# Performance work log

Measured on AMD Instinct MI355X. Metric: run time of the kernel, lower is better.

The kernel has to match this reference:

```python
import jax, jax.numpy as jnp
import numpy as np

N, E, H, DE = 50000, 800000, 128, 16

def silu(x):
    return x * jax.nn.sigmoid(x)

def setup_inputs() -> dict:
    key = jax.random.key(0)
    ks = jax.random.split(key, 24)
    def W(k, i, o, s=0.02):
        return (jax.random.normal(k, (i, o), jnp.float32) * s)
    inp = {
        'h': jax.random.normal(ks[0], (N, H), jnp.float32),
        'coord': jax.random.normal(ks[1], (N, 3), jnp.float32),
        'edge_index': jax.random.randint(ks[2], (2, E), 0, N),
        'edge_attr': jax.random.normal(ks[3], (E, DE), jnp.float32),
        # mes_mlp: Linear(2H+1+DE -> H), SiLU, Linear(H -> H), SiLU
        'mes_w1': W(ks[4], 2 * H + 1 + DE, H), 'mes_b1': jnp.zeros((H,), jnp.float32),
        'mes_w2': W(ks[5], H, H),              'mes_b2': jnp.zeros((H,), jnp.float32),
        # edge_mlp: Linear(H+1+DE -> H), SiLU, Linear(H -> H)
        'edge_w1': W(ks[6], H + 1 + DE, H),    'edge_b1': jnp.zeros((H,), jnp.float32),
        'edge_w2': W(ks[7], H, H),             'edge_b2': jnp.zeros((H,), jnp.float32),
        # node_mlp: Linear(H+H -> H), SiLU, Linear(H -> H)
        'node_w1': W(ks[8], 2 * H, H),         'node_b1': jnp.zeros((H,), jnp.float32),
        'node_w2': W(ks[9], H, H),             'node_b2': jnp.zeros((H,), jnp.float32),
        # coord_mlp: Linear(H -> H), SiLU, Linear(H -> 1, no bias, xavier gain 0.001)
        'coord_w1': W(ks[10], H, H),           'coord_b1': jnp.zeros((H,), jnp.float32),
        'coord_w2': W(ks[11], H, 1, s=0.001),
    }
    return inp

def reference(h, coord, edge_index, edge_attr,
              mes_w1, mes_b1, mes_w2, mes_b2,
              edge_w1, edge_b1, edge_w2, edge_b2,
              node_w1, node_b1, node_w2, node_b2,
              coord_w1, coord_b1, coord_w2):
    row, col = edge_index[0], edge_index[1]
    n = h.shape[0]
    # coord2radial
    coord_diff = coord[row] - coord[col]                        # [E,3]
    radial = jnp.sum(coord_diff ** 2, axis=1, keepdims=True)    # [E,1]
    norm = jnp.sqrt(radial + 1e-8)
    coord_diff = coord_diff / (norm + 1.0)
    # mes_model
    mes_in = jnp.concatenate([h[row], h[col], radial, edge_attr], axis=1)
    edge_feat = silu(silu(mes_in @ mes_w1 + mes_b1) @ mes_w2 + mes_b2)  # [E,H]
    # coord_model (agg='sum', no tanh)
    trans = coord_diff * (silu(edge_feat @ coord_w1 + coord_b1) @ coord_w2)  # [E,3]
    coord = coord + jax.ops.segment_sum(trans, col, num_segments=n)
    # node_model (recurrent)
    agg = jax.ops.segment_sum(edge_feat, col, num_segments=n)   # [N,H]
    node_in = jnp.concatenate([h, agg], axis=1)
    h = h + (silu(node_in @ node_w1 + node_b1) @ node_w2 + node_b2)
    # edge_model
    edge_in = jnp.concatenate([edge_feat, radial, edge_attr], axis=1)
    edge_out = silu(edge_in @ edge_w1 + edge_b1) @ edge_w2 + edge_b2
    return (h, coord, edge_out)
```

## Files before the change

kernel.cpp:

```cpp
#include <hip/hip_runtime.h>
#include <cstdint>
#include <cstddef>

typedef float f32x4 __attribute__((ext_vector_type(4)));
typedef __bf16 bf16x8 __attribute__((ext_vector_type(8)));
typedef unsigned short u16;

#define Hdim 128
#define DEdim 16
#define APITCH 296
#define FOFF   136
#define NPITCH 264

__device__ __forceinline__ u16 f2bf(float f){
  uint32_t u = __builtin_bit_cast(uint32_t, f);
  u += 0x7fffu + ((u >> 16) & 1u);
  return (u16)(u >> 16);
}
__device__ __forceinline__ uint32_t pack_bf2(float a, float b){
  return (uint32_t)f2bf(a) | ((uint32_t)f2bf(b) << 16);
}
__device__ __forceinline__ float bf2f(uint32_t lo16){
  return __builtin_bit_cast(float, lo16 << 16);
}
__device__ __forceinline__ float silu_f(float x){
  return x / (1.0f + __expf(-x));
}

template<int KC>
__device__ __forceinline__ void gemm_tile(
    const u16* A, int apitch,
    const u16* __restrict__ Bt, int kpad,
    const float* __restrict__ bias,
    int wv, int cidx, int hi, f32x4 (&acc)[4][2])
{
  const int c0 = (wv*2+0)*16 + cidx;
  const int c1 = (wv*2+1)*16 + cidx;
  const float b0 = bias[c0];
  const float b1 = bias[c1];
  #pragma unroll
  for (int rt=0; rt<4; ++rt){
    acc[rt][0] = (f32x4){b0,b0,b0,b0};
    acc[rt][1] = (f32x4){b1,b1,b1,b1};
  }
  #pragma unroll
  for (int kc=0; kc<KC; ++kc){
    const int ko = kc*32 + hi*8;
    bf16x8 bb0 = *(const bf16x8*)(Bt + (size_t)c0*kpad + ko);
    bf16x8 bb1 = *(const bf16x8*)(Bt + (size_t)c1*kpad + ko);
    #pragma unroll
    for (int rt=0; rt<4; ++rt){
      bf16x8 a = *(const bf16x8*)(A + (rt*16+cidx)*apitch + ko);
      acc[rt][0] = __builtin_amdgcn_mfma_f32_16x16x32_bf16(a, bb0, acc[rt][0], 0,0,0);
      acc[rt][1] = __builtin_amdgcn_mfma_f32_16x16x32_bf16(a, bb1, acc[rt][1], 0,0,0);
    }
  }
}

template<bool GATHER>
__global__ __launch_bounds__(256, 4) void egcl_edge(
    const float* __restrict__ h, const float* __restrict__ coord,
    const int* __restrict__ ei, const float* __restrict__ ea,
    const float* __restrict__ mes_b1, const float* __restrict__ mes_b2,
    const float* __restrict__ edge_b1, const float* __restrict__ edge_b2,
    const float* __restrict__ coord_b1, const float* __restrict__ coord_w2,
    const u16* __restrict__ w_mes1t, const u16* __restrict__ w_mes2t,
    const u16* __restrict__ w_coord1t, const u16* __restrict__ w_edge1t,
    const u16* __restrict__ w_edge2t,
    float* __restrict__ agg, u16* __restrict__ feat,
    float* __restrict__ out_coord, float* __restrict__ out_edge, int E, int N)
{
  __shared__ u16 Ab[64*APITCH];
  __shared__ float cds[64*4];
  __shared__ float tvs[64];
  __shared__ int cnode[64];

  const int tid  = threadIdx.x;
  const int lane = tid & 63;
  const int wv   = tid >> 6;
  const int e0   = blockIdx.x * 64;
  const int cidx = lane & 15;
  const int hi   = lane >> 4;

  {
    const int le   = wv*16 + (lane>>2);
    const int part = lane & 3;
    int eg = e0 + le;
    if (eg >= E) eg = E-1;
    const int node = (part < 2) ? ei[eg] : ei[E + eg];
    const float* src = h + (size_t)node*Hdim + (part&1)*64;
    u16* dst = Ab + le*APITCH + part*64;
    #pragma unroll
    for (int j=0;j<16;++j){
      const float4 v = ((const float4*)src)[j];
      ushort4 o; o.x=f2bf(v.x); o.y=f2bf(v.y); o.z=f2bf(v.z); o.w=f2bf(v.w);
      *(ushort4*)(dst + j*4) = o;
    }
    if (part == 0){
      const int cn = ei[E + eg];
      const float dx = coord[(size_t)node*3+0] - coord[(size_t)cn*3+0];
      const float dy = coord[(size_t)node*3+1] - coord[(size_t)cn*3+1];
      const float dz = coord[(size_t)node*3+2] - coord[(size_t)cn*3+2];
      const float radial = dx*dx + dy*dy + dz*dz;
      const float inv = 1.0f/(sqrtf(radial + 1e-8f) + 1.0f);
      cds[le*4+0]=dx*inv; cds[le*4+1]=dy*inv; cds[le*4+2]=dz*inv; cds[le*4+3]=radial;
      cnode[le] = cn;
      Ab[le*APITCH + 256] = f2bf(radial);
      #pragma unroll
      for (int j=0;j<DEdim;++j)
        Ab[le*APITCH + 257 + j] = f2bf(ea[(size_t)eg*DEdim + j]);
      #pragma unroll
      for (int j=273;j<288;++j) Ab[le*APITCH + j] = 0;
    }
    if (tid < 64) tvs[tid] = 0.f;
  }
  __syncthreads();

  f32x4 acc[4][2];

  gemm_tile<9>(Ab, APITCH, w_mes1t, 288, mes_b1, wv, cidx, hi, acc);
  __syncthreads();
  #pragma unroll
  for (int rt=0; rt<4; ++rt)
    #pragma unroll
    for (int j=0;j<2;++j){
      const int col = (wv*2+j)*16 + cidx;
      #pragma unroll
      for (int i=0;i<4;++i)
        Ab[(rt*16 + hi*4 + i)*APITCH + col] = f2bf(silu_f(acc[rt][j][i]));
    }
  if (tid < 64){
    const int row = tid;
    int eg = e0 + row; if (eg >= E) eg = E-1;
    Ab[row*APITCH + FOFF + 128] = f2bf(cds[row*4+3]);
    const float4* eap = (const float4*)(ea + (size_t)eg*DEdim);
    #pragma unroll
    for (int j=0;j<4;++j){
      const float4 v = eap[j];
      Ab[row*APITCH + FOFF + 129 + j*4 + 0] = f2bf(v.x);
      Ab[row*APITCH + FOFF + 129 + j*4 + 1] = f2bf(v.y);
      Ab[row*APITCH + FOFF + 129 + j*4 + 2] = f2bf(v.z);
      Ab[row*APITCH + FOFF + 129 + j*4 + 3] = f2bf(v.w);
    }
    #pragma unroll
    for (int j=145;j<160;++j) Ab[row*APITCH + FOFF + j] = 0;
  }
  __syncthreads();

  gemm_tile<4>(Ab, APITCH, w_mes2t, 128, mes_b2, wv, cidx, hi, acc);
  #pragma unroll
  for (int rt=0; rt<4; ++rt)
    #pragma unroll
    for (int j=0;j<2;++j){
      const int col = (wv*2+j)*16 + cidx;
      #pragma unroll
      for (int i=0;i<4;++i){
        const int row = rt*16 + hi*4 + i;
        const float v = silu_f(acc[rt][j][i]);
        if (!GATHER && e0 + row < E)
          atomicAdd(agg + (size_t)cnode[row]*Hdim + col, v);
        Ab[row*APITCH + FOFF + col] = f2bf(v);
      }
    }
  __syncthreads();

  if (GATHER){
    const int row = tid >> 2, seg = tid & 3;
    if (e0 + row < E){
      const int4* s = (const int4*)(Ab + row*APITCH + FOFF + seg*32);
      int4* d = (int4*)(feat + (size_t)(e0+row)*Hdim + seg*32);
      d[0]=s[0]; d[1]=s[1]; d[2]=s[2]; d[3]=s[3];
    }
  }

  gemm_tile<4>(Ab + FOFF, APITCH, w_coord1t, 128, coord_b1, wv, cidx, hi, acc);
  {
    const float cw0 = coord_w2[(wv*2+0)*16 + cidx];
    const float cw1 = coord_w2[(wv*2+1)*16 + cidx];
    #pragma unroll
    for (int rt=0; rt<4; ++rt)
      #pragma unroll
      for (int i=0;i<4;++i){
        float p = silu_f(acc[rt][0][i])*cw0 + silu_f(acc[rt][1][i])*cw1;
        p += __shfl_xor(p, 1);
        p += __shfl_xor(p, 2);
        p += __shfl_xor(p, 4);
        p += __shfl_xor(p, 8);
        if (cidx == 0) atomicAdd(&tvs[rt*16 + hi*4 + i], p);
      }
  }
  __syncthreads();
  if (tid < 192){
    const int le = tid/3, d = tid%3;
    if (e0 + le < E)
      atomicAdd(out_coord + (size_t)cnode[le]*3 + d, cds[le*4+d]*tvs[le]);
  }

  gemm_tile<5>(Ab + FOFF, APITCH, w_edge1t, 160, edge_b1, wv, cidx, hi, acc);
  #pragma unroll
  for (int rt=0; rt<4; ++rt)
    #pragma unroll
    for (int j=0;j<2;++j){
      const int col = (wv*2+j)*16 + cidx;
      #pragma unroll
      for (int i=0;i<4;++i)
        Ab[(rt*16 + hi*4 + i)*APITCH + col] = f2bf(silu_f(acc[rt][j][i]));
    }
  __syncthreads();

  gemm_tile<4>(Ab, APITCH, w_edge2t, 128, edge_b2, wv, cidx, hi, acc);
  #pragma unroll
  for (int rt=0; rt<4; ++rt)
    #pragma unroll
    for (int j=0;j<2;++j){
      const int col = (wv*2+j)*16 + cidx;
      #pragma unroll
      for (int i=0;i<4;++i){
        const int row = rt*16 + hi*4 + i;
        const int eg = e0 + row;
        if (eg < E) out_edge[(size_t)eg*Hdim + col] = acc[rt][j][i];
      }
    }
}

template<bool GATHER>
__global__ __launch_bounds__(256, 4) void egcl_node(
    const float* __restrict__ h, const float* __restrict__ agg,
    const int* __restrict__ offs, const int* __restrict__ deg,
    const int* __restrict__ elist, const u16* __restrict__ feat,
    const float* __restrict__ node_b1, const float* __restrict__ node_b2,
    const u16* __restrict__ w_node1t, const u16* __restrict__ w_node2t,
    float* __restrict__ out_h, int N)
{
  __shared__ u16 Ab[64*NPITCH];
  const int tid  = threadIdx.x;
  const int lane = tid & 63;
  const int wv   = tid >> 6;
  const int r0   = blockIdx.x * 64;
  const int cidx = lane & 15;
  const int hi   = lane >> 4;

  {
    const int le   = wv*16 + (lane>>2);
    const int part = lane & 3;
    int g = r0 + le;
    if (g >= N) g = N-1;
    const float* src = h + (size_t)g*Hdim + part*32;
    u16* dst = Ab + le*NPITCH + part*32;
    #pragma unroll
    for (int j=0;j<8;++j){
      const float4 v = ((const float4*)src)[j];
      ushort4 o; o.x=f2bf(v.x); o.y=f2bf(v.y); o.z=f2bf(v.z); o.w=f2bf(v.w);
      *(ushort4*)(dst + j*4) = o;
    }
  }
  if (GATHER){
    const uint32_t* fp = (const uint32_t*)feat;
    for (int ln=0; ln<16; ++ln){
      const int le = wv*16 + ln;
      const int g = r0 + le;
      float a0 = 0.f, a1 = 0.f;
      if (g < N){
        const int start = __builtin_amdgcn_readfirstlane(offs[g]);
        const int dg    = __builtin_amdgcn_readfirstlane(deg[g]);
        int d = 0;
        for (; d + 4 <= dg; d += 4){
          const int e0 = elist[start+d+0];
          const int e1 = elist[start+d+1];
          const int e2 = elist[start+d+2];
          const int e3 = elist[start+d+3];
          const uint32_t v0 = fp[(size_t)e0*64 + lane];
          const uint32_t v1 = fp[(size_t)e1*64 + lane];
          const uint32_t v2 = fp[(size_t)e2*64 + lane];
          const uint32_t v3 = fp[(size_t)e3*64 + lane];
          a0 += bf2f(v0 & 0xffffu) + bf2f(v1 & 0xffffu) + bf2f(v2 & 0xffffu) + bf2f(v3 & 0xffffu);
          a1 += bf2f(v0 >> 16)     + bf2f(v1 >> 16)     + bf2f(v2 >> 16)     + bf2f(v3 >> 16);
        }
        for (; d < dg; ++d){
          const int e = elist[start+d];
          const uint32_t v = fp[(size_t)e*64 + lane];
          a0 += bf2f(v & 0xffffu);
          a1 += bf2f(v >> 16);
        }
      }
      *(uint32_t*)&Ab[(size_t)le*NPITCH + 128 + lane*2] = pack_bf2(a0, a1);
    }
  } else {
    const int le   = wv*16 + (lane>>2);
    const int part = lane & 3;
    int g = r0 + le;
    if (g >= N) g = N-1;
    const float* src = agg + (size_t)g*Hdim + part*32;
    u16* dst = Ab + le*NPITCH + 128 + part*32;
    #pragma unroll
    for (int j=0;j<8;++j){
      const float4 v = ((const float4*)src)[j];
      ushort4 o; o.x=f2bf(v.x); o.y=f2bf(v.y); o.z=f2bf(v.z); o.w=f2bf(v.w);
      *(ushort4*)(dst + j*4) = o;
    }
  }
  __syncthreads();

  f32x4 acc[4][2];
  gemm_tile<8>(Ab, NPITCH, w_node1t, 256, node_b1, wv, cidx, hi, acc);
  __syncthreads();
  #pragma unroll
  for (int rt=0; rt<4; ++rt)
    #pragma unroll
    for (int j=0;j<2;++j){
      const int col = (wv*2+j)*16 + cidx;
      #pragma unroll
      for (int i=0;i<4;++i)
        Ab[(rt*16 + hi*4 + i)*NPITCH + col] = f2bf(silu_f(acc[rt][j][i]));
    }
  __syncthreads();
  gemm_tile<4>(Ab, NPITCH, w_node2t, 128, node_b2, wv, cidx, hi, acc);
  #pragma unroll
  for (int rt=0; rt<4; ++rt)
    #pragma unroll
    for (int j=0;j<2;++j){
      const int col = (wv*2+j)*16 + cidx;
      #pragma unroll
      for (int i=0;i<4;++i){
        const int row = rt*16 + hi*4 + i;
        const int g = r0 + row;
        if (g < N)
          out_h[(size_t)g*Hdim + col] = h[(size_t)g*Hdim + col] + acc[rt][j][i];
      }
    }
}

__global__ void egcl_init(const float* __restrict__ coord, float* __restrict__ out_coord,
                          int nc, float* __restrict__ zf, int nzf,
                          int* __restrict__ zi, int nzi)
{
  const int i = blockIdx.x*256 + threadIdx.x;
  if (i < nc)   out_coord[i] = coord[i];
  if (zf && i < nzf) zf[i] = 0.f;
  if (zi && i < nzi) zi[i] = 0;
}

__global__ void egcl_wconv(const float* __restrict__ src, u16* __restrict__ dst,
                           int K, int Kpad)
{
  const int i = blockIdx.x*256 + threadIdx.x;
  if (i >= 128*Kpad) return;
  const int c = i / Kpad, k = i - c*Kpad;
  const float v = (k < K) ? src[(size_t)k*128 + c] : 0.f;
  dst[i] = f2bf(v);
}

__global__ void k_hist(const int* __restrict__ ei, int* __restrict__ hist, int E){
  const int i = blockIdx.x*256 + threadIdx.x;
  if (i < E) atomicAdd(&hist[ei[E + i]], 1);
}
__global__ void k_scan1(const int* __restrict__ hist, int* __restrict__ partial, int N){
  __shared__ int s[256];
  const int t = threadIdx.x, i = blockIdx.x*256 + t;
  s[t] = (i < N) ? hist[i] : 0;
  __syncthreads();
  for (int o=128; o>0; o>>=1){ if (t < o) s[t] += s[t+o]; __syncthreads(); }
  if (t == 0) partial[blockIdx.x] = s[0];
}
__global__ void k_scan2(int* __restrict__ partial, int G){
  if (blockIdx.x == 0 && threadIdx.x == 0){
    int run = 0;
    for (int i=0;i<G;++i){ const int v = partial[i]; partial[i] = run; run += v; }
  }
}
__global__ void k_scan3(const int* __restrict__ hist, const int* __restrict__ partial,
                        int* __restrict__ offs, int* __restrict__ cursor, int N){
  __shared__ int s[256];
  const int t = threadIdx.x, i = blockIdx.x*256 + t;
  const int v = (i < N) ? hist[i] : 0;
  s[t] = v;
  __syncthreads();
  for (int o=1; o<256; o<<=1){
    int x = (t >= o) ? s[t-o] : 0;
    __syncthreads();
    s[t] += x;
    __syncthreads();
  }
  const int ex = s[t] - v + partial[blockIdx.x];
  if (i < N){ offs[i] = ex; cursor[i] = ex; }
}
__global__ void k_scatter(const int* __restrict__ ei, int* __restrict__ cursor,
                          int* __restrict__ elist, int E){
  const int i = blockIdx.x*256 + threadIdx.x;
  if (i < E){
    const int c = ei[E + i];
    const int p = atomicAdd(&cursor[c], 1);
    elist[p] = i;
  }
}

extern "C" void kernel_launch(void* const* d_in, const int* in_sizes, int n_in,
                              void* d_out, int out_size, void* d_ws, size_t ws_size,
                              hipStream_t stream)
{
  const float* h       = (const float*)d_in[0];
  const float* coord   = (const float*)d_in[1];
  const int*   ei      = (const int*)d_in[2];
  const float* ea      = (const float*)d_in[3];
  const float* mes_w1  = (const float*)d_in[4];
  const float* mes_b1  = (const float*)d_in[5];
  const float* mes_w2  = (const float*)d_in[6];
  const float* mes_b2  = (const float*)d_in[7];
  const float* edge_w1 = (const float*)d_in[8];
  const float* edge_b1 = (const float*)d_in[9];
  const float* edge_w2 = (const float*)d_in[10];
  const float* edge_b2 = (const float*)d_in[11];
  const float* node_w1 = (const float*)d_in[12];
  const float* node_b1 = (const float*)d_in[13];
  const float* node_w2 = (const float*)d_in[14];
  const float* node_b2 = (const float*)d_in[15];
  const float* coord_w1= (const float*)d_in[16];
  const float* coord_b1= (const float*)d_in[17];
  const float* coord_w2= (const float*)d_in[18];

  const int N = in_sizes[0] / Hdim;
  const int E = in_sizes[2] / 2;
  const int G1 = (N + 255) / 256;

  char* ws = (char*)d_ws;
  u16* w_mes1t    = (u16*)ws;
  u16* w_mes2t    = w_mes1t  + 128*288;
  u16* w_coord1t  = w_mes2t  + 128*128;
  u16* w_edge1t   = w_coord1t+ 128*128;
  u16* w_edge2t   = w_edge1t + 128*160;
  u16* w_node1t   = w_edge2t + 128*128;
  u16* w_node2t   = w_node1t + 128*256;
  const size_t woff = (((size_t)(288+128+128+160+128+256+128)*128*2) + 255) & ~(size_t)255;

  auto align256 = [](size_t x){ return (x + 255) & ~(size_t)255; };
  const size_t o_feat  = woff;
  const size_t o_hist  = o_feat + align256((size_t)E*Hdim*2);
  const size_t o_offs  = o_hist + align256((size_t)N*4);
  const size_t o_cur   = o_offs + align256((size_t)N*4);
  const size_t o_part  = o_cur  + align256((size_t)N*4);
  const size_t o_elist = o_part + align256((size_t)G1*4);
  const size_t need    = o_elist + (size_t)E*4;
  const bool gather = (ws_size >= need);

  float* out_h     = (float*)d_out;
  float* out_coord = out_h + (size_t)N*Hdim;
  float* out_edge  = out_coord + (size_t)N*3;

  egcl_wconv<<<(128*288 + 255)/256, 256, 0, stream>>>(mes_w1,   w_mes1t,   2*Hdim+1+DEdim, 288);
  egcl_wconv<<<(128*128 + 255)/256, 256, 0, stream>>>(mes_w2,   w_mes2t,   128, 128);
  egcl_wconv<<<(128*128 + 255)/256, 256, 0, stream>>>(coord_w1, w_coord1t, 128, 128);
  egcl_wconv<<<(128*160 + 255)/256, 256, 0, stream>>>(edge_w1,  w_edge1t,  Hdim+1+DEdim, 160);
  egcl_wconv<<<(128*128 + 255)/256, 256, 0, stream>>>(edge_w2,  w_edge2t,  128, 128);
  egcl_wconv<<<(128*256 + 255)/256, 256, 0, stream>>>(node_w1,  w_node1t,  256, 256);
  egcl_wconv<<<(128*128 + 255)/256, 256, 0, stream>>>(node_w2,  w_node2t,  128, 128);

  if (gather){
    u16* feat   = (u16*)(ws + o_feat);
    int* hist   = (int*)(ws + o_hist);
    int* offs   = (int*)(ws + o_offs);
    int* cursor = (int*)(ws + o_cur);
    int* partial= (int*)(ws + o_part);
    int* elist  = (int*)(ws + o_elist);

    egcl_init<<<(N*3 > N ? (N*3+255)/256 : (N+255)/256), 256, 0, stream>>>(
        coord, out_coord, N*3, nullptr, 0, hist, N);
    k_hist<<<(E + 255)/256, 256, 0, stream>>>(ei, hist, E);
    k_scan1<<<G1, 256, 0, stream>>>(hist, partial, N);
    k_scan2<<<1, 64, 0, stream>>>(partial, G1);
    k_scan3<<<G1, 256, 0, stream>>>(hist, partial, offs, cursor, N);
    k_scatter<<<(E + 255)/256, 256, 0, stream>>>(ei, cursor, elist, E);

    egcl_edge<true><<<(E + 63)/64, 256, 0, stream>>>(h, coord, ei, ea,
        mes_b1, mes_b2, edge_b1, edge_b2, coord_b1, coord_w2,
        w_mes1t, w_mes2t, w_coord1t, w_edge1t, w_edge2t,
        nullptr, feat, out_coord, out_edge, E, N);

    egcl_node<true><<<(N + 63)/64, 256, 0, stream>>>(h, nullptr, offs, hist, elist, feat,
        node_b1, node_b2, w_node1t, w_node2t, out_h, N);
  } else {
    float* agg = (float*)(ws + woff);
    egcl_init<<<(N*Hdim + 255)/256, 256, 0, stream>>>(
        coord, out_coord, N*3, agg, N*Hdim, nullptr, 0);

    egcl_edge<false><<<(E + 63)/64, 256, 0, stream>>>(h, coord, ei, ea,
        mes_b1, mes_b2, edge_b1, edge_b2, coord_b1, coord_w2,
        w_mes1t, w_mes2t, w_coord1t, w_edge1t, w_edge2t,
        agg, nullptr, out_coord, out_edge, E, N);

    egcl_node<false><<<(N + 63)/64, 256, 0, stream>>>(h, agg, nullptr, nullptr, nullptr, nullptr,
        node_b1, node_b2, w_node1t, w_node2t, out_h, N);
  }
}
```

Measured before the change: 718.2 us.

## Precompute per-node first-layer projections and restructure edge kernel GEMM layout

Splits the first message-MLP layer algebraically: h@W_row and h@W_col are computed once per node (N rows) in a new projection kernel, and each edge just adds the two bf16 projections instead of running a 256-wide GEMM per edge. The edge kernel is reworked with swapped MFMA operands, a separate small tile for radial/edge_attr, vectorized bf16 stores, and a smaller shared buffer that raises the occupancy hint. Edge features are written in CSR-sorted position so the node kernel reads them contiguously, and the seven weight-conversion launches are merged into one. The cost is an extra N x 256 bf16 workspace, one more rounding of the projected sums to bf16, and a larger, riskier rewrite.

```diff
diff --git a/kernel.cpp b/kernel.cpp
--- a/kernel.cpp
+++ b/kernel.cpp
@@ -4,76 +4,110 @@
 
 typedef float f32x4 __attribute__((ext_vector_type(4)));
 typedef __bf16 bf16x8 __attribute__((ext_vector_type(8)));
+typedef __bf16 bf16x4 __attribute__((ext_vector_type(4)));
+typedef __bf16 bf16x2 __attribute__((ext_vector_type(2)));
 typedef unsigned short u16;
 
 #define Hdim 128
 #define DEdim 16
-#define APITCH 296
-#define FOFF   136
-#define NPITCH 264
-
-__device__ __forceinline__ u16 f2bf(float f){
-  uint32_t u = __builtin_bit_cast(uint32_t, f);
-  u += 0x7fffu + ((u >> 16) & 1u);
-  return (u16)(u >> 16);
-}
-__device__ __forceinline__ uint32_t pack_bf2(float a, float b){
-  return (uint32_t)f2bf(a) | ((uint32_t)f2bf(b) << 16);
-}
+#define TP 40
+
 __device__ __forceinline__ float bf2f(uint32_t lo16){
   return __builtin_bit_cast(float, lo16 << 16);
 }
+__device__ __forceinline__ float bfhi(uint32_t v){
+  return __builtin_bit_cast(float, v & 0xffff0000u);
+}
 __device__ __forceinline__ float silu_f(float x){
   return x / (1.0f + __expf(-x));
 }
+__device__ __forceinline__ uint32_t addbf2(uint32_t a, uint32_t b){
+  float lo = bf2f(a & 0xffffu) + bf2f(b & 0xffffu);
+  float hi = bfhi(a) + bfhi(b);
+  bf16x2 p; p[0] = (__bf16)lo; p[1] = (__bf16)hi;
+  return __builtin_bit_cast(uint32_t, p);
+}
+__device__ __forceinline__ uint2 pack4(f32x4 v){
+  bf16x4 p;
+  #pragma unroll
+  for (int i=0;i<4;++i) p[i] = (__bf16)v[i];
+  return __builtin_bit_cast(uint2, p);
+}
+__device__ __forceinline__ uint2 silu_pack4(const f32x4& v, f32x4* sout=nullptr){
+  f32x4 s;
+  #pragma unroll
+  for (int i=0;i<4;++i) s[i] = silu_f(v[i]);
+  if (sout) *sout = s;
+  return pack4(s);
+}
 
 template<int KC>
-__device__ __forceinline__ void gemm_tile(
+__device__ __forceinline__ void gemm_sw(
     const u16* A, int apitch,
-    const u16* __restrict__ Bt, int kpad,
-    const float* __restrict__ bias,
+    const u16* __restrict__ Wt, int kpad, int woff,
     int wv, int cidx, int hi, f32x4 (&acc)[4][2])
 {
-  const int c0 = (wv*2+0)*16 + cidx;
-  const int c1 = (wv*2+1)*16 + cidx;
-  const float b0 = bias[c0];
-  const float b1 = bias[c1];
-  #pragma unroll
-  for (int rt=0; rt<4; ++rt){
-    acc[rt][0] = (f32x4){b0,b0,b0,b0};
-    acc[rt][1] = (f32x4){b1,b1,b1,b1};
-  }
+  const u16* w0p = Wt + (size_t)((wv*2+0)*16 + cidx)*kpad + woff + hi*8;
+  const u16* w1p = Wt + (size_t)((wv*2+1)*16 + cidx)*kpad + woff + hi*8;
+  const u16* ap  = A + (size_t)cidx*apitch + hi*8;
   #pragma unroll
   for (int kc=0; kc<KC; ++kc){
-    const int ko = kc*32 + hi*8;
-    bf16x8 bb0 = *(const bf16x8*)(Bt + (size_t)c0*kpad + ko);
-    bf16x8 bb1 = *(const bf16x8*)(Bt + (size_t)c1*kpad + ko);
-    #pragma unroll
-    for (int rt=0; rt<4; ++rt){
-      bf16x8 a = *(const bf16x8*)(A + (rt*16+cidx)*apitch + ko);
-      acc[rt][0] = __builtin_amdgcn_mfma_f32_16x16x32_bf16(a, bb0, acc[rt][0], 0,0,0);
-      acc[rt][1] = __builtin_amdgcn_mfma_f32_16x16x32_bf16(a, bb1, acc[rt][1], 0,0,0);
-    }
-  }
-}
-
-template<bool GATHER>
-__global__ __launch_bounds__(256, 4) void egcl_edge(
+    bf16x8 w0 = *(const bf16x8*)(w0p + kc*32);
+    bf16x8 w1 = *(const bf16x8*)(w1p + kc*32);
+    #pragma unroll
+    for (int et=0; et<4; ++et){
+      bf16x8 a = *(const bf16x8*)(ap + et*16*apitch + kc*32);
+      acc[et][0] = __builtin_amdgcn_mfma_f32_16x16x32_bf16(w0, a, acc[et][0], 0,0,0);
+      acc[et][1] = __builtin_amdgcn_mfma_f32_16x16x32_bf16(w1, a, acc[et][1], 0,0,0);
+    }
+  }
+}
+
+__device__ __forceinline__ void acc_bias(const float* __restrict__ bias,
+                                         int wv, int hi, f32x4 (&acc)[4][2])
+{
+  f32x4 b0 = *(const f32x4*)(bias + (wv*2+0)*16 + hi*4);
+  f32x4 b1 = *(const f32x4*)(bias + (wv*2+1)*16 + hi*4);
+  #pragma unroll
+  for (int et=0;et<4;++et){ acc[et][0]=b0; acc[et][1]=b1; }
+}
+
+template<int SP>
+__device__ __forceinline__ void write_silu_S(u16* S, f32x4 (&acc)[4][2],
+                                             int wv, int cidx, int hi)
+{
+  #pragma unroll
+  for (int et=0; et<4; ++et){
+    const int e = et*16 + cidx;
+    #pragma unroll
+    for (int j=0;j<2;++j){
+      const int f0 = (wv*2+j)*16 + hi*4;
+      *(uint2*)(S + (size_t)e*SP + f0) = silu_pack4(acc[et][j]);
+    }
+  }
+}
+
+template<bool PROJ, bool GATHER>
+__global__ __launch_bounds__(256, PROJ?6:3) void egcl_edge(
     const float* __restrict__ h, const float* __restrict__ coord,
     const int* __restrict__ ei, const float* __restrict__ ea,
+    const u16* __restrict__ proj, const int* __restrict__ pos,
     const float* __restrict__ mes_b1, const float* __restrict__ mes_b2,
     const float* __restrict__ edge_b1, const float* __restrict__ edge_b2,
     const float* __restrict__ coord_b1, const float* __restrict__ coord_w2,
     const u16* __restrict__ w_mes1t, const u16* __restrict__ w_mes2t,
     const u16* __restrict__ w_coord1t, const u16* __restrict__ w_edge1t,
     const u16* __restrict__ w_edge2t,
-    float* __restrict__ agg, u16* __restrict__ feat,
-    float* __restrict__ out_coord, float* __restrict__ out_edge, int E, int N)
-{
-  __shared__ u16 Ab[64*APITCH];
+    float* __restrict__ agg, u16* __restrict__ featb,
+    float* __restrict__ out_coord, float* __restrict__ out_edge, int E)
+{
+  constexpr int SP = PROJ ? 136 : 264;
+  __shared__ u16 S[64*SP];
+  __shared__ u16 T[64*TP];
   __shared__ float cds[64*4];
-  __shared__ float tvs[64];
+  __shared__ float tvs[4][64];
   __shared__ int cnode[64];
+  __shared__ int epos[64];
 
   const int tid  = threadIdx.x;
   const int lane = tid & 63;
@@ -85,249 +119,290 @@
   {
     const int le   = wv*16 + (lane>>2);
     const int part = lane & 3;
-    int eg = e0 + le;
-    if (eg >= E) eg = E-1;
-    const int node = (part < 2) ? ei[eg] : ei[E + eg];
-    const float* src = h + (size_t)node*Hdim + (part&1)*64;
-    u16* dst = Ab + le*APITCH + part*64;
-    #pragma unroll
-    for (int j=0;j<16;++j){
-      const float4 v = ((const float4*)src)[j];
-      ushort4 o; o.x=f2bf(v.x); o.y=f2bf(v.y); o.z=f2bf(v.z); o.w=f2bf(v.w);
-      *(ushort4*)(dst + j*4) = o;
+    int eg = e0 + le; if (eg >= E) eg = E-1;
+    const int rn = ei[eg], cn = ei[E + eg];
+    if constexpr (PROJ){
+      const uint4* pr = (const uint4*)(proj + (size_t)rn*256 + part*32);
+      const uint4* pc = (const uint4*)(proj + (size_t)cn*256 + 128 + part*32);
+      u16* dst = S + (size_t)le*SP + part*32;
+      #pragma unroll
+      for (int q=0;q<4;++q){
+        uint4 a = pr[q], b = pc[q], o;
+        o.x = addbf2(a.x, b.x); o.y = addbf2(a.y, b.y);
+        o.z = addbf2(a.z, b.z); o.w = addbf2(a.w, b.w);
+        *(uint4*)(dst + q*8) = o;
+      }
+    } else {
+      const float* src = ((part<2) ? h + (size_t)rn*Hdim : h + (size_t)cn*Hdim) + (part&1)*64;
+      u16* dst = S + (size_t)le*SP + part*64;
+      #pragma unroll
+      for (int q=0;q<16;++q){
+        float4 v = ((const float4*)src)[q];
+        bf16x4 o = {(__bf16)v.x,(__bf16)v.y,(__bf16)v.z,(__bf16)v.w};
+        *(bf16x4*)(dst + q*4) = o;
+      }
     }
     if (part == 0){
-      const int cn = ei[E + eg];
-      const float dx = coord[(size_t)node*3+0] - coord[(size_t)cn*3+0];
-      const float dy = coord[(size_t)node*3+1] - coord[(size_t)cn*3+1];
-      const float dz = coord[(size_t)node*3+2] - coord[(size_t)cn*3+2];
+      cnode[le] = cn;
+      if constexpr (GATHER) epos[le] = pos[eg];
+      const float dx = coord[(size_t)rn*3+0] - coord[(size_t)cn*3+0];
+      const float dy = coord[(size_t)rn*3+1] - coord[(size_t)cn*3+1];
+      const float dz = coord[(size_t)rn*3+2] - coord[(size_t)cn*3+2];
       const float radial = dx*dx + dy*dy + dz*dz;
       const float inv = 1.0f/(sqrtf(radial + 1e-8f) + 1.0f);
       cds[le*4+0]=dx*inv; cds[le*4+1]=dy*inv; cds[le*4+2]=dz*inv; cds[le*4+3]=radial;
-      cnode[le] = cn;
-      Ab[le*APITCH + 256] = f2bf(radial);
-      #pragma unroll
-      for (int j=0;j<DEdim;++j)
-        Ab[le*APITCH + 257 + j] = f2bf(ea[(size_t)eg*DEdim + j]);
-      #pragma unroll
-      for (int j=273;j<288;++j) Ab[le*APITCH + j] = 0;
-    }
-    if (tid < 64) tvs[tid] = 0.f;
+      u16* tp = T + le*TP;
+      const float4* eap = (const float4*)(ea + (size_t)eg*DEdim);
+      #pragma unroll
+      for (int q=0;q<4;++q){
+        float4 v = eap[q];
+        bf16x4 o = {(__bf16)v.x,(__bf16)v.y,(__bf16)v.z,(__bf16)v.w};
+        *(bf16x4*)(tp + q*4) = o;
+      }
+      bf16x4 z = {(__bf16)0.f,(__bf16)0.f,(__bf16)0.f,(__bf16)0.f};
+      *(bf16x4*)(tp+16) = z; *(bf16x4*)(tp+20) = z;
+      *(bf16x4*)(tp+24) = z; *(bf16x4*)(tp+28) = z;
+      *(__bf16*)(tp+16) = (__bf16)radial;
+    }
+    ((float*)tvs)[tid] = 0.f;
   }
   __syncthreads();
 
   f32x4 acc[4][2];
 
-  gemm_tile<9>(Ab, APITCH, w_mes1t, 288, mes_b1, wv, cidx, hi, acc);
-  __syncthreads();
-  #pragma unroll
-  for (int rt=0; rt<4; ++rt)
+  acc_bias(mes_b1, wv, hi, acc);
+  if constexpr (PROJ){
+    #pragma unroll
+    for (int et=0;et<4;++et){
+      const int e = et*16 + cidx;
+      #pragma unroll
+      for (int j=0;j<2;++j){
+        const int f0 = (wv*2+j)*16 + hi*4;
+        ushort4 sv = *(const ushort4*)(S + (size_t)e*SP + f0);
+        acc[et][j][0] += bf2f(sv.x); acc[et][j][1] += bf2f(sv.y);
+        acc[et][j][2] += bf2f(sv.z); acc[et][j][3] += bf2f(sv.w);
+      }
+    }
+    gemm_sw<1>(T, TP, w_mes1t, 288, 256, wv, cidx, hi, acc);
+  } else {
+    gemm_sw<8>(S, SP, w_mes1t, 288, 0,   wv, cidx, hi, acc);
+    gemm_sw<1>(T, TP, w_mes1t, 288, 256, wv, cidx, hi, acc);
+    __syncthreads();
+  }
+  write_silu_S<SP>(S, acc, wv, cidx, hi);
+  __syncthreads();
+
+  acc_bias(mes_b2, wv, hi, acc);
+  gemm_sw<4>(S, SP, w_mes2t, 128, 0, wv, cidx, hi, acc);
+  uint2 ps[4][2];
+  #pragma unroll
+  for (int et=0;et<4;++et)
     #pragma unroll
     for (int j=0;j<2;++j){
-      const int col = (wv*2+j)*16 + cidx;
-      #pragma unroll
-      for (int i=0;i<4;++i)
-        Ab[(rt*16 + hi*4 + i)*APITCH + col] = f2bf(silu_f(acc[rt][j][i]));
-    }
-  if (tid < 64){
-    const int row = tid;
-    int eg = e0 + row; if (eg >= E) eg = E-1;
-    Ab[row*APITCH + FOFF + 128] = f2bf(cds[row*4+3]);
-    const float4* eap = (const float4*)(ea + (size_t)eg*DEdim);
-    #pragma unroll
-    for (int j=0;j<4;++j){
-      const float4 v = eap[j];
-      Ab[row*APITCH + FOFF + 129 + j*4 + 0] = f2bf(v.x);
-      Ab[row*APITCH + FOFF + 129 + j*4 + 1] = f2bf(v.y);
-      Ab[row*APITCH + FOFF + 129 + j*4 + 2] = f2bf(v.z);
-      Ab[row*APITCH + FOFF + 129 + j*4 + 3] = f2bf(v.w);
-    }
-    #pragma unroll
-    for (int j=145;j<160;++j) Ab[row*APITCH + FOFF + j] = 0;
-  }
-  __syncthreads();
-
-  gemm_tile<4>(Ab, APITCH, w_mes2t, 128, mes_b2, wv, cidx, hi, acc);
-  #pragma unroll
-  for (int rt=0; rt<4; ++rt)
-    #pragma unroll
-    for (int j=0;j<2;++j){
-      const int col = (wv*2+j)*16 + cidx;
-      #pragma unroll
-      for (int i=0;i<4;++i){
-        const int row = rt*16 + hi*4 + i;
-        const float v = silu_f(acc[rt][j][i]);
-        if (!GATHER && e0 + row < E)
-          atomicAdd(agg + (size_t)cnode[row]*Hdim + col, v);
-        Ab[row*APITCH + FOFF + col] = f2bf(v);
-      }
-    }
-  __syncthreads();
-
-  if (GATHER){
+      f32x4 sv;
+      ps[et][j] = silu_pack4(acc[et][j], &sv);
+      if constexpr (!GATHER){
+        const int e = et*16 + cidx;
+        if (e0 + e < E){
+          const int f0 = (wv*2+j)*16 + hi*4;
+          #pragma unroll
+          for (int i=0;i<4;++i)
+            atomicAdd(agg + (size_t)cnode[e]*Hdim + f0 + i, sv[i]);
+        }
+      }
+    }
+  __syncthreads();
+  #pragma unroll
+  for (int et=0;et<4;++et)
+    #pragma unroll
+    for (int j=0;j<2;++j)
+      *(uint2*)(S + (size_t)(et*16+cidx)*SP + (wv*2+j)*16 + hi*4) = ps[et][j];
+  __syncthreads();
+
+  if constexpr (GATHER){
     const int row = tid >> 2, seg = tid & 3;
     if (e0 + row < E){
-      const int4* s = (const int4*)(Ab + row*APITCH + FOFF + seg*32);
-      int4* d = (int4*)(feat + (size_t)(e0+row)*Hdim + seg*32);
+      const int4* s = (const int4*)(S + (size_t)row*SP + seg*32);
+      int4* d = (int4*)(featb + (size_t)epos[row]*Hdim + seg*32);
       d[0]=s[0]; d[1]=s[1]; d[2]=s[2]; d[3]=s[3];
     }
   }
 
-  gemm_tile<4>(Ab + FOFF, APITCH, w_coord1t, 128, coord_b1, wv, cidx, hi, acc);
+  acc_bias(coord_b1, wv, hi, acc);
+  gemm_sw<4>(S, SP, w_coord1t, 128, 0, wv, cidx, hi, acc);
   {
-    const float cw0 = coord_w2[(wv*2+0)*16 + cidx];
-    const float cw1 = coord_w2[(wv*2+1)*16 + cidx];
-    #pragma unroll
-    for (int rt=0; rt<4; ++rt)
-      #pragma unroll
-      for (int i=0;i<4;++i){
-        float p = silu_f(acc[rt][0][i])*cw0 + silu_f(acc[rt][1][i])*cw1;
-        p += __shfl_xor(p, 1);
-        p += __shfl_xor(p, 2);
-        p += __shfl_xor(p, 4);
-        p += __shfl_xor(p, 8);
-        if (cidx == 0) atomicAdd(&tvs[rt*16 + hi*4 + i], p);
-      }
-  }
+    f32x4 cw0 = *(const f32x4*)(coord_w2 + (wv*2+0)*16 + hi*4);
+    f32x4 cw1 = *(const f32x4*)(coord_w2 + (wv*2+1)*16 + hi*4);
+    #pragma unroll
+    for (int et=0;et<4;++et){
+      float p = 0.f;
+      #pragma unroll
+      for (int i=0;i<4;++i)
+        p += silu_f(acc[et][0][i])*cw0[i] + silu_f(acc[et][1][i])*cw1[i];
+      p += __shfl_xor(p, 16);
+      p += __shfl_xor(p, 32);
+      if (hi == 0) tvs[wv][et*16+cidx] = p;
+    }
+  }
+
+  acc_bias(edge_b1, wv, hi, acc);
+  gemm_sw<4>(S, SP, w_edge1t, 160, 0,   wv, cidx, hi, acc);
+  gemm_sw<1>(T, TP, w_edge1t, 160, 128, wv, cidx, hi, acc);
+  #pragma unroll
+  for (int et=0;et<4;++et)
+    #pragma unroll
+    for (int j=0;j<2;++j)
+      ps[et][j] = silu_pack4(acc[et][j]);
   __syncthreads();
   if (tid < 192){
-    const int le = tid/3, d = tid%3;
-    if (e0 + le < E)
-      atomicAdd(out_coord + (size_t)cnode[le]*3 + d, cds[le*4+d]*tvs[le]);
-  }
-
-  gemm_tile<5>(Ab + FOFF, APITCH, w_edge1t, 160, edge_b1, wv, cidx, hi, acc);
-  #pragma unroll
-  for (int rt=0; rt<4; ++rt)
-    #pragma unroll
-    for (int j=0;j<2;++j){
-      const int col = (wv*2+j)*16 + cidx;
-      #pragma unroll
-      for (int i=0;i<4;++i)
-        Ab[(rt*16 + hi*4 + i)*APITCH + col] = f2bf(silu_f(acc[rt][j][i]));
-    }
-  __syncthreads();
-
-  gemm_tile<4>(Ab, APITCH, w_edge2t, 128, edge_b2, wv, cidx, hi, acc);
-  #pragma unroll
-  for (int rt=0; rt<4; ++rt)
-    #pragma unroll
-    for (int j=0;j<2;++j){
-      const int col = (wv*2+j)*16 + cidx;
-      #pragma unroll
-      for (int i=0;i<4;++i){
-        const int row = rt*16 + hi*4 + i;
-        const int eg = e0 + row;
-        if (eg < E) out_edge[(size_t)eg*Hdim + col] = acc[rt][j][i];
-      }
-    }
+    const int le = tid/3, d = tid - le*3;
+    if (e0 + le < E){
+      const float t4 = tvs[0][le]+tvs[1][le]+tvs[2][le]+tvs[3][le];
+      atomicAdd(out_coord + (size_t)cnode[le]*3 + d, cds[le*4+d]*t4);
+    }
+  }
+  #pragma unroll
+  for (int et=0;et<4;++et)
+    #pragma unroll
+    for (int j=0;j<2;++j)
+      *(uint2*)(S + (size_t)(et*16+cidx)*SP + (wv*2+j)*16 + hi*4) = ps[et][j];
+  __syncthreads();
+
+  acc_bias(edge_b2, wv, hi, acc);
+  gemm_sw<4>(S, SP, w_edge2t, 128, 0, wv, cidx, hi, acc);
+  #pragma unroll
+  for (int et=0;et<4;++et){
+    const int e = e0 + et*16 + cidx;
+    if (e < E){
+      #pragma unroll
+      for (int j=0;j<2;++j)
+        *(f32x4*)(out_edge + (size_t)e*Hdim + (wv*2+j)*16 + hi*4) = acc[et][j];
+    }
+  }
+}
+
+__global__ __launch_bounds__(256, 6) void egcl_proj(
+    const float* __restrict__ h, const u16* __restrict__ w_mes1t,
+    u16* __restrict__ proj, int N)
+{
+  __shared__ u16 S[64*136];
+  const int tid=threadIdx.x, lane=tid&63, wv=tid>>6, cidx=lane&15, hi=lane>>4;
+  const int r0 = blockIdx.x*64, half = blockIdx.y;
+  {
+    const int le = tid>>2, part = tid&3;
+    int g = r0 + le; if (g >= N) g = N-1;
+    const float* src = h + (size_t)g*Hdim + part*32;
+    u16* dst = S + (size_t)le*136 + part*32;
+    #pragma unroll
+    for (int q=0;q<8;++q){
+      float4 v = ((const float4*)src)[q];
+      bf16x4 o = {(__bf16)v.x,(__bf16)v.y,(__bf16)v.z,(__bf16)v.w};
+      *(bf16x4*)(dst + q*4) = o;
+    }
+  }
+  __syncthreads();
+  f32x4 acc[4][2];
+  #pragma unroll
+  for (int et=0;et<4;++et){ acc[et][0]=(f32x4){0,0,0,0}; acc[et][1]=(f32x4){0,0,0,0}; }
+  gemm_sw<4>(S, 136, w_mes1t, 288, half*128, wv, cidx, hi, acc);
+  #pragma unroll
+  for (int et=0;et<4;++et){
+    const int g = r0 + et*16 + cidx;
+    if (g < N){
+      #pragma unroll
+      for (int j=0;j<2;++j)
+        *(uint2*)(proj + (size_t)g*256 + half*128 + (wv*2+j)*16 + hi*4) = pack4(acc[et][j]);
+    }
+  }
 }
 
 template<bool GATHER>
 __global__ __launch_bounds__(256, 4) void egcl_node(
     const float* __restrict__ h, const float* __restrict__ agg,
     const int* __restrict__ offs, const int* __restrict__ deg,
-    const int* __restrict__ elist, const u16* __restrict__ feat,
+    const u16* __restrict__ featb,
     const float* __restrict__ node_b1, const float* __restrict__ node_b2,
     const u16* __restrict__ w_node1t, const u16* __restrict__ w_node2t,
     float* __restrict__ out_h, int N)
 {
-  __shared__ u16 Ab[64*NPITCH];
-  const int tid  = threadIdx.x;
-  const int lane = tid & 63;
-  const int wv   = tid >> 6;
-  const int r0   = blockIdx.x * 64;
-  const int cidx = lane & 15;
-  const int hi   = lane >> 4;
-
+  __shared__ u16 Ab[64*264];
+  const int tid=threadIdx.x, lane=tid&63, wv=tid>>6, cidx=lane&15, hi=lane>>4;
+  const int r0 = blockIdx.x*64;
   {
-    const int le   = wv*16 + (lane>>2);
-    const int part = lane & 3;
-    int g = r0 + le;
-    if (g >= N) g = N-1;
+    const int le = tid>>2, part = tid&3;
+    int g = r0 + le; if (g >= N) g = N-1;
     const float* src = h + (size_t)g*Hdim + part*32;
-    u16* dst = Ab + le*NPITCH + part*32;
-    #pragma unroll
-    for (int j=0;j<8;++j){
-      const float4 v = ((const float4*)src)[j];
-      ushort4 o; o.x=f2bf(v.x); o.y=f2bf(v.y); o.z=f2bf(v.z); o.w=f2bf(v.w);
-      *(ushort4*)(dst + j*4) = o;
-    }
-  }
-  if (GATHER){
-    const uint32_t* fp = (const uint32_t*)feat;
-    for (int ln=0; ln<16; ++ln){
-      const int le = wv*16 + ln;
-      const int g = r0 + le;
-      float a0 = 0.f, a1 = 0.f;
-      if (g < N){
-        const int start = __builtin_amdgcn_readfirstlane(offs[g]);
-        const int dg    = __builtin_amdgcn_readfirstlane(deg[g]);
-        int d = 0;
-        for (; d + 4 <= dg; d += 4){
-          const int e0 = elist[start+d+0];
-          const int e1 = elist[start+d+1];
-          const int e2 = elist[start+d+2];
-          const int e3 = elist[start+d+3];
-          const uint32_t v0 = fp[(size_t)e0*64 + lane];
-          const uint32_t v1 = fp[(size_t)e1*64 + lane];
-          const uint32_t v2 = fp[(size_t)e2*64 + lane];
-          const uint32_t v3 = fp[(size_t)e3*64 + lane];
-          a0 += bf2f(v0 & 0xffffu) + bf2f(v1 & 0xffffu) + bf2f(v2 & 0xffffu) + bf2f(v3 & 0xffffu);
-          a1 += bf2f(v0 >> 16)     + bf2f(v1 >> 16)     + bf2f(v2 >> 16)     + bf2f(v3 >> 16);
+    u16* dst = Ab + (size_t)le*264 + part*32;
+    #pragma unroll
+    for (int q=0;q<8;++q){
+      float4 v = ((const float4*)src)[q];
+      bf16x4 o = {(__bf16)v.x,(__bf16)v.y,(__bf16)v.z,(__bf16)v.w};
+      *(bf16x4*)(dst + q*4) = o;
+    }
+  }
+  if constexpr (GATHER){
+    const int le = tid>>2, part = tid&3;
+    const int g = r0 + le;
+    float a[32];
+    #pragma unroll
+    for (int q=0;q<32;++q) a[q]=0.f;
+    if (g < N){
+      const int s = offs[g], dg = deg[g];
+      const u16* base = featb + (size_t)s*Hdim + part*32;
+      #pragma unroll 2
+      for (int r=0;r<dg;++r){
+        const uint4* rp = (const uint4*)(base + (size_t)r*Hdim);
+        #pragma unroll
+        for (int q=0;q<4;++q){
+          uint4 w = rp[q];
+          a[q*8+0] += bf2f(w.x & 0xffffu); a[q*8+1] += bfhi(w.x);
+          a[q*8+2] += bf2f(w.y & 0xffffu); a[q*8+3] += bfhi(w.y);
+          a[q*8+4] += bf2f(w.z & 0xffffu); a[q*8+5] += bfhi(w.z);
+          a[q*8+6] += bf2f(w.w & 0xffffu); a[q*8+7] += bfhi(w.w);
         }
-        for (; d < dg; ++d){
-          const int e = elist[start+d];
-          const uint32_t v = fp[(size_t)e*64 + lane];
-          a0 += bf2f(v & 0xffffu);
-          a1 += bf2f(v >> 16);
-        }
-      }
-      *(uint32_t*)&Ab[(size_t)le*NPITCH + 128 + lane*2] = pack_bf2(a0, a1);
+      }
+    }
+    u16* dst = Ab + (size_t)le*264 + 128 + part*32;
+    #pragma unroll
+    for (int q=0;q<8;++q){
+      bf16x4 o = {(__bf16)a[q*4+0],(__bf16)a[q*4+1],(__bf16)a[q*4+2],(__bf16)a[q*4+3]};
+      *(bf16x4*)(dst + q*4) = o;
     }
   } else {
-    const int le   = wv*16 + (lane>>2);
-    const int part = lane & 3;
-    int g = r0 + le;
-    if (g >= N) g = N-1;
+    const int le = tid>>2, part = tid&3;
+    int g = r0 + le; if (g >= N) g = N-1;
     const float* src = agg + (size_t)g*Hdim + part*32;
-    u16* dst = Ab + le*NPITCH + 128 + part*32;
-    #pragma unroll
-    for (int j=0;j<8;++j){
-      const float4 v = ((const float4*)src)[j];
-      ushort4 o; o.x=f2bf(v.x); o.y=f2bf(v.y); o.z=f2bf(v.z); o.w=f2bf(v.w);
-      *(ushort4*)(dst + j*4) = o;
+    u16* dst = Ab + (size_t)le*264 + 128 + part*32;
+    #pragma unroll
+    for (int q=0;q<8;++q){
+      float4 v = ((const float4*)src)[q];
+      bf16x4 o = {(__bf16)v.x,(__bf16)v.y,(__bf16)v.z,(__bf16)v.w};
+      *(bf16x4*)(dst + q*4) = o;
     }
   }
   __syncthreads();
 
   f32x4 acc[4][2];
-  gemm_tile<8>(Ab, NPITCH, w_node1t, 256, node_b1, wv, cidx, hi, acc);
-  __syncthreads();
-  #pragma unroll
-  for (int rt=0; rt<4; ++rt)
-    #pragma unroll
-    for (int j=0;j<2;++j){
-      const int col = (wv*2+j)*16 + cidx;
-      #pragma unroll
-      for (int i=0;i<4;++i)
-        Ab[(rt*16 + hi*4 + i)*NPITCH + col] = f2bf(silu_f(acc[rt][j][i]));
-    }
-  __syncthreads();
-  gemm_tile<4>(Ab, NPITCH, w_node2t, 128, node_b2, wv, cidx, hi, acc);
-  #pragma unroll
-  for (int rt=0; rt<4; ++rt)
-    #pragma unroll
-    for (int j=0;j<2;++j){
-      const int col = (wv*2+j)*16 + cidx;
-      #pragma unroll
-      for (int i=0;i<4;++i){
-        const int row = rt*16 + hi*4 + i;
-        const int g = r0 + row;
-        if (g < N)
-          out_h[(size_t)g*Hdim + col] = h[(size_t)g*Hdim + col] + acc[rt][j][i];
-      }
-    }
+  acc_bias(node_b1, wv, hi, acc);
+  gemm_sw<8>(Ab, 264, w_node1t, 256, 0, wv, cidx, hi, acc);
+  __syncthreads();
+  write_silu_S<264>(Ab, acc, wv, cidx, hi);
+  __syncthreads();
+  acc_bias(node_b2, wv, hi, acc);
+  gemm_sw<4>(Ab, 264, w_node2t, 128, 0, wv, cidx, hi, acc);
+  #pragma unroll
+  for (int et=0;et<4;++et){
+    const int g = r0 + et*16 + cidx;
+    if (g < N){
+      #pragma unroll
+      for (int j=0;j<2;++j){
+        const int f0 = (wv*2+j)*16 + hi*4;
+        f32x4 hv = *(const f32x4*)(h + (size_t)g*Hdim + f0);
+        hv += acc[et][j];
+        *(f32x4*)(out_h + (size_t)g*Hdim + f0) = hv;
+      }
+    }
+  }
 }
 
 __global__ void egcl_init(const float* __restrict__ coord, float* __restrict__ out_coord,
@@ -335,19 +410,37 @@
                           int* __restrict__ zi, int nzi)
 {
   const int i = blockIdx.x*256 + threadIdx.x;
-  if (i < nc)   out_coord[i] = coord[i];
+  if (i < nc) out_coord[i] = coord[i];
   if (zf && i < nzf) zf[i] = 0.f;
   if (zi && i < nzi) zi[i] = 0;
 }
 
-__global__ void egcl_wconv(const float* __restrict__ src, u16* __restrict__ dst,
-                           int K, int Kpad)
-{
-  const int i = blockIdx.x*256 + threadIdx.x;
-  if (i >= 128*Kpad) return;
-  const int c = i / Kpad, k = i - c*Kpad;
-  const float v = (k < K) ? src[(size_t)k*128 + c] : 0.f;
-  dst[i] = f2bf(v);
+__global__ void egcl_wconv7(
+    const float* s0, const float* s1, const float* s2, const float* s3,
+    const float* s4, const float* s5, const float* s6, u16* __restrict__ dst)
+{
+  static const int kpads[7]  = {288,128,128,160,128,256,128};
+  static const int Ks[7]     = {273,128,128,145,128,256,128};
+  static const int modes[7]  = {1,0,0,2,0,0,0};
+  const int gi = blockIdx.x*256 + threadIdx.x;
+  int w = 0, off = 0, boff = 0;
+  #pragma unroll
+  for (int t=0;t<7;++t){
+    const int sz = 128*kpads[t];
+    if (gi >= off && gi < off + sz){ w = t; boff = off; }
+    off += sz;
+  }
+  if (gi >= off) return;
+  const float* srcs[7] = {s0,s1,s2,s3,s4,s5,s6};
+  const int li = gi - boff;
+  const int kpad = kpads[w], K = Ks[w], mode = modes[w];
+  const int c = li / kpad, k = li - c*kpad;
+  int ks;
+  if (mode==1)      ks = (k<256) ? k : (k<272 ? k+1 : (k==272 ? 256 : -1));
+  else if (mode==2) ks = (k<128) ? k : (k<144 ? k+1 : (k==144 ? 128 : -1));
+  else              ks = (k<K) ? k : -1;
+  const float v = (ks>=0) ? srcs[w][(size_t)ks*128 + c] : 0.f;
+  *(__bf16*)(dst + gi) = (__bf16)v;
 }
 
 __global__ void k_hist(const int* __restrict__ ei, int* __restrict__ hist, int E){
@@ -385,12 +478,11 @@
   if (i < N){ offs[i] = ex; cursor[i] = ex; }
 }
 __global__ void k_scatter(const int* __restrict__ ei, int* __restrict__ cursor,
-                          int* __restrict__ elist, int E){
+                          int* __restrict__ pos, int E){
   const int i = blockIdx.x*256 + threadIdx.x;
   if (i < E){
     const int c = ei[E + i];
-    const int p = atomicAdd(&cursor[c], 1);
-    elist[p] = i;
+    pos[i] = atomicAdd(&cursor[c], 1);
   }
 }
 
@@ -423,71 +515,77 @@
   const int G1 = (N + 255) / 256;
 
   char* ws = (char*)d_ws;
-  u16* w_mes1t    = (u16*)ws;
-  u16* w_mes2t    = w_mes1t  + 128*288;
-  u16* w_coord1t  = w_mes2t  + 128*128;
-  u16* w_edge1t   = w_coord1t+ 128*128;
-  u16* w_edge2t   = w_edge1t + 128*160;
-  u16* w_node1t   = w_edge2t + 128*128;
-  u16* w_node2t   = w_node1t + 128*256;
-  const size_t woff = (((size_t)(288+128+128+160+128+256+128)*128*2) + 255) & ~(size_t)255;
-
-  auto align256 = [](size_t x){ return (x + 255) & ~(size_t)255; };
-  const size_t o_feat  = woff;
-  const size_t o_hist  = o_feat + align256((size_t)E*Hdim*2);
-  const size_t o_offs  = o_hist + align256((size_t)N*4);
-  const size_t o_cur   = o_offs + align256((size_t)N*4);
-  const size_t o_part  = o_cur  + align256((size_t)N*4);
-  const size_t o_elist = o_part + align256((size_t)G1*4);
-  const size_t need    = o_elist + (size_t)E*4;
-  const bool gather = (ws_size >= need);
+  const size_t wtot = (size_t)(288+128+128+160+128+256+128)*128;
+  u16* wbase     = (u16*)ws;
+  u16* w_mes1t   = wbase;
+  u16* w_mes2t   = w_mes1t  + 128*288;
+  u16* w_coord1t = w_mes2t  + 128*128;
+  u16* w_edge1t  = w_coord1t+ 128*128;
+  u16* w_edge2t  = w_edge1t + 128*160;
+  u16* w_node1t  = w_edge2t + 128*128;
+  u16* w_node2t  = w_node1t + 128*256;
+
+  auto al = [](size_t x){ return (x + 255) & ~(size_t)255; };
+  const size_t base   = al(wtot*2);
+  const size_t o_feat = base;
+  const size_t o_hist = o_feat + al((size_t)E*Hdim*2);
+  const size_t o_offs = o_hist + al((size_t)N*4);
+  const size_t o_cur  = o_offs + al((size_t)N*4);
+  const size_t o_part = o_cur  + al((size_t)N*4);
+  const size_t o_pos  = o_part + al((size_t)G1*4);
+  const size_t gather_end = o_pos + al((size_t)E*4);
+  const size_t o_proj = gather_end;
+  const size_t proj_end = o_proj + (size_t)N*256*2;
+  const bool gather = (ws_size >= gather_end);
+  const bool proj   = (ws_size >= proj_end);
 
   float* out_h     = (float*)d_out;
   float* out_coord = out_h + (size_t)N*Hdim;
   float* out_edge  = out_coord + (size_t)N*3;
 
-  egcl_wconv<<<(128*288 + 255)/256, 256, 0, stream>>>(mes_w1,   w_mes1t,   2*Hdim+1+DEdim, 288);
-  egcl_wconv<<<(128*128 + 255)/256, 256, 0, stream>>>(mes_w2,   w_mes2t,   128, 128);
-  egcl_wconv<<<(128*128 + 255)/256, 256, 0, stream>>>(coord_w1, w_coord1t, 128, 128);
-  egcl_wconv<<<(128*160 + 255)/256, 256, 0, stream>>>(edge_w1,  w_edge1t,  Hdim+1+DEdim, 160);
-  egcl_wconv<<<(128*128 + 255)/256, 256, 0, stream>>>(edge_w2,  w_edge2t,  128, 128);
-  egcl_wconv<<<(128*256 + 255)/256, 256, 0, stream>>>(node_w1,  w_node1t,  256, 256);
-  egcl_wconv<<<(128*128 + 255)/256, 256, 0, stream>>>(node_w2,  w_node2t,  128, 128);
+  const int wblocks = (int)((wtot + 255)/256);
+  egcl_wconv7<<<wblocks, 256, 0, stream>>>(mes_w1, mes_w2, coord_w1, edge_w1,
+                                           edge_w2, node_w1, node_w2, wbase);
 
   if (gather){
-    u16* feat   = (u16*)(ws + o_feat);
+    u16* featb  = (u16*)(ws + o_feat);
     int* hist   = (int*)(ws + o_hist);
     int* offs   = (int*)(ws + o_offs);
     int* cursor = (int*)(ws + o_cur);
     int* partial= (int*)(ws + o_part);
-    int* elist  = (int*)(ws + o_elist);
-
-    egcl_init<<<(N*3 > N ? (N*3+255)/256 : (N+255)/256), 256, 0, stream>>>(
-        coord, out_coord, N*3, nullptr, 0, hist, N);
-    k_hist<<<(E + 255)/256, 256, 0, stream>>>(ei, hist, E);
+    int* pos    = (int*)(ws + o_pos);
+    u16* projp  = (u16*)(ws + o_proj);
+
+    egcl_init<<<(N*3+255)/256, 256, 0, stream>>>(coord, out_coord, N*3, nullptr, 0, hist, N);
+    k_hist<<<(E+255)/256, 256, 0, stream>>>(ei, hist, E);
     k_scan1<<<G1, 256, 0, stream>>>(hist, partial, N);
     k_scan2<<<1, 64, 0, stream>>>(partial, G1);
     k_scan3<<<G1, 256, 0, stream>>>(hist, partial, offs, cursor, N);
-    k_scatter<<<(E + 255)/256, 256, 0, stream>>>(ei, cursor, elist, E);
-
-    egcl_edge<true><<<(E + 63)/64, 256, 0, stream>>>(h, coord, ei, ea,
+    k_scatter<<<(E+255)/256, 256, 0, stream>>>(ei, cursor, pos, E);
+
+    if (proj){
+      dim3 pg((N+63)/64, 2);
+      egcl_proj<<<pg, 256, 0, stream>>>(h, w_mes1t, projp, N);
+      egcl_edge<true,true><<<(E+63)/64, 256, 0, stream>>>(h, coord, ei, ea, projp, pos,
+          mes_b1, mes_b2, edge_b1, edge_b2, coord_b1, coord_w2,
+          w_mes1t, w_mes2t, w_coord1t, w_edge1t, w_edge2t,
+          nullptr, featb, out_coord, out_edge, E);
+    } else {
+      egcl_edge<false,true><<<(E+63)/64, 256, 0, stream>>>(h, coord, ei, ea, nullptr, pos,
+          mes_b1, mes_b2, edge_b1, edge_b2, coord_b1, coord_w2,
+          w_mes1t, w_mes2t, w_coord1t, w_edge1t, w_edge2t,
+          nullptr, featb, out_coord, out_edge, E);
+    }
+    egcl_node<true><<<(N+63)/64, 256, 0, stream>>>(h, nullptr, offs, hist, featb,
+        node_b1, node_b2, w_node1t, w_node2t, out_h, N);
+  } else {
+    float* agg = (float*)(ws + base);
+    egcl_init<<<(N*Hdim+255)/256, 256, 0, stream>>>(coord, out_coord, N*3, agg, N*Hdim, nullptr, 0);
+    egcl_edge<false,false><<<(E+63)/64, 256, 0, stream>>>(h, coord, ei, ea, nullptr, nullptr,
         mes_b1, mes_b2, edge_b1, edge_b2, coord_b1, coord_w2,
         w_mes1t, w_mes2t, w_coord1t, w_edge1t, w_edge2t,
-        nullptr, feat, out_coord, out_edge, E, N);
-
-    egcl_node<true><<<(N + 63)/64, 256, 0, stream>>>(h, nullptr, offs, hist, elist, feat,
+        agg, nullptr, out_coord, out_edge, E);
+    egcl_node<false><<<(N+63)/64, 256, 0, stream>>>(h, agg, nullptr, nullptr, nullptr,
         node_b1, node_b2, w_node1t, w_node2t, out_h, N);
-  } else {
-    float* agg = (float*)(ws + woff);
-    egcl_init<<<(N*Hdim + 255)/256, 256, 0, stream>>>(
-        coord, out_coord, N*3, agg, N*Hdim, nullptr, 0);
-
-    egcl_edge<false><<<(E + 63)/64, 256, 0, stream>>>(h, coord, ei, ea,
-        mes_b1, mes_b2, edge_b1, edge_b2, coord_b1, coord_w2,
-        w_mes1t, w_mes2t, w_coord1t, w_edge1t, w_edge2t,
-        agg, nullptr, out_coord, out_edge, E, N);
-
-    egcl_node<false><<<(N + 63)/64, 256, 0, stream>>>(h, agg, nullptr, nullptr, nullptr, nullptr,
-        node_b1, node_b2, w_node1t, w_node2t, out_h, N);
-  }
-}
+  }
+}
```

Result: slower. 864.6 us (+20.4%).
